# Kernel tuning notes

Hardware: AMD Instinct MI355X
Metric: run time of the kernel (lower is better)

## Reference

```python
import jax, jax.numpy as jnp
import numpy as np

CC_ITERS = 60  # min-label propagation + pointer doubling; covers huge diameters


def setup_inputs() -> dict:
    key = jax.random.key(0)
    k1, k2, k3, k4, k5 = jax.random.split(key, 5)
    N, C, E = 100000, 128, 800000
    x = jax.random.normal(k1, (N, C), jnp.float32)
    src = jax.random.randint(k2, (E,), 0, N)
    off = jax.random.randint(k3, (E,), 1, N)
    dst = (src + off) % N  # guarantees no self-loops (torch forward filters them)
    edge_index = jnp.stack([src, dst]).astype(jnp.int32)
    batch = jnp.zeros((N,), jnp.int32)
    W = jax.random.normal(k4, (2 * C,), jnp.float32) * 0.05
    b = (jax.random.normal(k5, (), jnp.float32) * 0.05).astype(jnp.float32)
    return {"x": x, "edge_index": edge_index, "batch": batch, "W": W, "b": b}


def _connected_components(src, dst, mask, N):
    # min-label propagation along selected edges, with path compression.
    def body(i, labels):
        ls = jnp.where(mask, labels[src], N)
        ld = jnp.where(mask, labels[dst], N)
        new = labels.at[dst].min(ls).at[src].min(ld)
        return jnp.minimum(new, new[new])  # pointer doubling
    return jax.lax.fori_loop(0, CC_ITERS, body, jnp.arange(N))


def reference(x, edge_index, batch, W, b):
    N, C = x.shape
    E = edge_index.shape[1]
    src, dst = edge_index[0], edge_index[1]

    # raw edge score: Linear(cat(x[src], x[dst])) without materializing the concat
    e = x[src] @ W[:C] + x[dst] @ W[C:] + b  # [E]
    # softmax over incoming edges of each dst node (segment softmax)
    m = jax.ops.segment_max(e, dst, num_segments=N)
    z = jnp.exp(e - m[dst])
    s = jax.ops.segment_sum(z, dst, num_segments=N)
    score = z / s[dst] + 0.5  # add_to_edge_score

    # edge selection (E > N -> quantile branch, matching torch)
    if E > N:
        q = 1.0 - (N // 2) / E
        mask = score > jnp.quantile(score, q)
    else:
        mask = score >= jnp.median(score)

    # weighted pairwise node reps for selected edges (masked instead of gathered)
    w = jnp.where(mask, score, 0.0)
    reps = (x[src] + x[dst]) * w[:, None]  # [E, C]
    mi = mask.astype(x.dtype)
    cnt = jnp.zeros((N,), x.dtype).at[src].add(mi).at[dst].add(mi)  # bincount of selected endpoints
    merged = cnt > 0
    base = jnp.where(merged[:, None], 0.0, x)  # merged nodes zeroed, untouched nodes keep x
    acc = base.at[src].add(reps).at[dst].add(reps)
    nodes = jnp.where(merged[:, None], acc / jnp.maximum(cnt, 1.0)[:, None], acc)

    # connected components over selected edges; relabel by first-occurrence order
    labels = _connected_components(src, dst, jax.lax.stop_gradient(mask), N)
    uniq = jnp.unique(labels, size=N, fill_value=N)
    cluster = jnp.searchsorted(uniq, labels)  # [N]

    new_x = jax.ops.segment_sum(nodes, cluster, num_segments=N)  # padded to N clusters

    # coalesce cluster-mapped edges: sorted unique pairs, padded with -1
    c0, c1 = cluster[src], cluster[dst]
    keys = jnp.unique(c0.astype(jnp.int64) * N + c1.astype(jnp.int64), size=E, fill_value=-1)
    valid = keys >= 0
    new_edge_index = jnp.stack([
        jnp.where(valid, keys // N, -1),
        jnp.where(valid, keys % N, -1),
    ])
    new_batch = jnp.zeros((N,), batch.dtype).at[cluster].set(batch)
    return new_x, new_edge_index, new_batch, score
```

## Files before the change

### kernel.cpp

```cpp
#include <hip/hip_runtime.h>
#include <math.h>
#include <stdint.h>

typedef unsigned long long u64;
typedef unsigned int u32;

#define NN 100000
#define CF 128
#define EE 800000

#define CAP 131072

#define EBITS 11
#define ERADIX 2048
#define ETILE 4096
#define NB_E 196
#define SORT_N (NB_E * ETILE)
#define MBITS 12
#define MRADIX 4096
#define MTILE 2048
#define NB_M 49
#define MSORT_N (NB_M * MTILE)
#define HISTG_LEN 401408

#define SCTILE 2048
#define MCHUNK 16

#define ZSCALE 4503599627370496.0
#define XSCALE 32768.0f
#define XINV   (1.0f / 32768.0f)

struct Sel { u32 prefix; u32 k; };

__device__ inline u64 encD(double v) {
  u64 u = (u64)__double_as_longlong(v);
  return u ^ ((u >> 63) ? ~0ULL : 0x8000000000000000ULL);
}
__device__ inline double decD(u64 u) {
  u ^= ((u >> 63) ? 0x8000000000000000ULL : ~0ULL);
  return __longlong_as_double((long long)u);
}

__global__ void k_pq(const float* __restrict__ x, const float* __restrict__ W,
                     double* __restrict__ p, double* __restrict__ q) {
  int node = blockIdx.x * 4 + (threadIdx.x >> 6);
  int lane = threadIdx.x & 63;
  if (node >= NN) return;
  const float* xr = x + (size_t)node * CF;
  double a = (double)xr[lane] * (double)W[lane] + (double)xr[lane + 64] * (double)W[lane + 64];
  double c = (double)xr[lane] * (double)W[CF + lane] + (double)xr[lane + 64] * (double)W[CF + lane + 64];
  for (int off = 32; off; off >>= 1) { a += __shfl_xor(a, off); c += __shfl_xor(c, off); }
  if (lane == 0) { p[node] = a; q[node] = c; }
}

__global__ void k_em(const int* __restrict__ ei, const double* __restrict__ p,
                     const double* __restrict__ q, const float* __restrict__ bptr,
                     double* __restrict__ e, u64* __restrict__ menc) {
  int j = blockIdx.x * 256 + threadIdx.x;
  if (j >= EE) return;
  int s = ei[j], d = ei[EE + j];
  double ev = p[s] + q[d] + (double)bptr[0];
  e[j] = ev;
  atomicMax(&menc[d], encD(ev));
}

__global__ void k_zs(const int* __restrict__ ei, double* __restrict__ e,
                     const u64* __restrict__ menc, u64* __restrict__ sdenFx) {
  int j = blockIdx.x * 256 + threadIdx.x;
  if (j >= EE) return;
  int d = ei[EE + j];
  double z = exp(e[j] - decD(menc[d]));
  e[j] = z;
  atomicAdd(&sdenFx[d], (u64)__double2ll_rn(z * ZSCALE));
}

__global__ void k_score(const int* __restrict__ ei, const double* __restrict__ z,
                        const u64* __restrict__ sdenFx, float* __restrict__ outScore) {
  int j = blockIdx.x * 256 + threadIdx.x;
  if (j >= EE) return;
  int d = ei[EE + j];
  double s = (double)sdenFx[d] * (1.0 / ZSCALE);
  outScore[j] = (float)(z[j] / s + 0.5);
}

__global__ void k_selInit(Sel* st, u32* hist, int k0, int k1) {
  int t = blockIdx.x * 256 + threadIdx.x;
  if (t == 0) { st[0].prefix = 0x3Fu; st[0].k = (u32)k0; st[1].prefix = 0x3Fu; st[1].k = (u32)k1; }
  if (t < 512) hist[t] = 0;
}

__global__ void k_selHist(const float* __restrict__ score, const Sel* __restrict__ st,
                          u32* __restrict__ hist, int shift) {
  __shared__ u32 h[512];
  for (int i = threadIdx.x; i < 512; i += 256) h[i] = 0;
  __syncthreads();
  u32 p0 = st[0].prefix, p1 = st[1].prefix;
  for (int j = blockIdx.x * 256 + threadIdx.x; j < EE; j += gridDim.x * 256) {
    u32 u = __float_as_uint(score[j]);
    u32 d = (u >> shift) & 255u;
    if ((u >> (shift + 8)) == p0) atomicAdd(&h[d], 1u);
    if ((u >> (shift + 8)) == p1) atomicAdd(&h[256 + d], 1u);
  }
  __syncthreads();
  for (int i = threadIdx.x; i < 512; i += 256) if (h[i]) atomicAdd(&hist[i], h[i]);
}

__global__ void k_selPick(Sel* st, u32* hist, float* tval, float frac, int last) {
  if (threadIdx.x == 0) {
    for (int sel = 0; sel < 2; sel++) {
      u32 k = st[sel].k, cum = 0;
      for (int b = 0; b < 256; b++) {
        u32 c = hist[sel * 256 + b];
        if (cum + c > k) { st[sel].prefix = (st[sel].prefix << 8) | (u32)b; st[sel].k = k - cum; break; }
        cum += c;
      }
    }
    if (last) {
      float a = __uint_as_float(st[0].prefix);
      float b = __uint_as_float(st[1].prefix);
      tval[0] = __fadd_rn(a, __fmul_rn(__fsub_rn(b, a), frac));
    }
  }
  __syncthreads();
  for (int i = threadIdx.x; i < 512; i += blockDim.x) hist[i] = 0;
}

__global__ void __launch_bounds__(1024) k_compact(
    const float* __restrict__ score, const float* __restrict__ tval,
    const int* __restrict__ ei, int* __restrict__ selCount,
    int* __restrict__ selSrc, int* __restrict__ selDst,
    float* __restrict__ selW, int* __restrict__ cnt, int* __restrict__ labels) {
  __shared__ int wbase[16];
  int j = blockIdx.x * 1024 + threadIdx.x;
  if (j < NN) labels[j] = j;
  int lane = threadIdx.x & 63;
  int wid = threadIdx.x >> 6;
  float sc = 0.0f;
  bool sel = false;
  if (j < EE) { sc = score[j]; sel = (sc > tval[0]); }
  u64 m = __ballot(sel);
  int wcnt = __popcll(m);
  int rank = __popcll(m & ((1ULL << lane) - 1ULL));
  if (lane == 0) wbase[wid] = wcnt;
  __syncthreads();
  if (threadIdx.x == 0) {
    int tot = 0;
#pragma unroll
    for (int w = 0; w < 16; w++) tot += wbase[w];
    int base = tot ? atomicAdd(selCount, tot) : 0;
#pragma unroll
    for (int w = 0; w < 16; w++) { int c = wbase[w]; wbase[w] = base; base += c; }
  }
  __syncthreads();
  if (sel) {
    int s = ei[j], d = ei[EE + j];
    int pos = wbase[wid] + rank;
    if (pos < CAP) { selSrc[pos] = s; selDst[pos] = d; selW[pos] = sc; }
    atomicAdd(&cnt[s], 1);
    atomicAdd(&cnt[d], 1);
  }
}

__device__ inline int uf_find(int* parent, int x) {
  while (true) {
    int p = parent[x];
    if (p == x) return x;
    int gp = parent[p];
    if (gp == p) return p;
    parent[x] = gp;
    x = gp;
  }
}

__global__ void k_ufUnion(const int* __restrict__ selSrc, const int* __restrict__ selDst,
                          const int* __restrict__ selCount, int* __restrict__ parent) {
  int n = selCount[0]; if (n > CAP) n = CAP;
  for (int e = blockIdx.x * 256 + threadIdx.x; e < n; e += gridDim.x * 256) {
    int ru = uf_find(parent, selSrc[e]);
    int rv = uf_find(parent, selDst[e]);
    while (ru != rv) {
      if (ru < rv) { int t = ru; ru = rv; rv = t; }
      int old = atomicCAS(&parent[ru], ru, rv);
      if (old == ru) break;
      ru = uf_find(parent, old);
      rv = uf_find(parent, rv);
    }
  }
}

__global__ void k_ufFlattenRoots(int* __restrict__ parent, int* __restrict__ roots) {
  int i = blockIdx.x * 256 + threadIdx.x;
  if (i >= NN) return;
  int x = i;
  while (true) { int p = parent[x]; if (p == x) break; x = p; }
  parent[i] = x;
  roots[i] = (x == i) ? 1 : 0;
}

__global__ void k_clusterMkeys(const int* __restrict__ labels, const int* __restrict__ rootScan,
                               int* __restrict__ cluster, u64* __restrict__ mkeys,
                               int* __restrict__ rootNode) {
  int i = blockIdx.x * 256 + threadIdx.x;
  if (i < NN) {
    int cl = rootScan[labels[i]];
    cluster[i] = cl;
    mkeys[i] = ((u64)(u32)cl << 32) | (u32)i;
    if (labels[i] == i) rootNode[cl] = i;
  } else if (i < MSORT_N) {
    mkeys[i] = ~0ULL;
  }
}

__global__ void k_scanBlock(const int* __restrict__ src, int* __restrict__ dst,
                            int n, int* __restrict__ bsums) {
  __shared__ int part[256];
  int base = blockIdx.x * SCTILE + threadIdx.x * 8;
  int v[8]; int s = 0;
#pragma unroll
  for (int i = 0; i < 8; i++) { v[i] = (base + i < n) ? src[base + i] : 0; s += v[i]; }
  part[threadIdx.x] = s;
  __syncthreads();
  for (int off = 1; off < 256; off <<= 1) {
    int t = (threadIdx.x >= off) ? part[threadIdx.x - off] : 0;
    __syncthreads();
    part[threadIdx.x] += t;
    __syncthreads();
  }
  int run = part[threadIdx.x] - s;
#pragma unroll
  for (int i = 0; i < 8; i++) { int vv = v[i]; if (base + i < n) dst[base + i] = run; run += vv; }
  if (threadIdx.x == 255) bsums[blockIdx.x] = part[255];
}
__global__ void k_scanFlags(const u32* __restrict__ keys, int* __restrict__ dst,
                            int n, int* __restrict__ bsums) {
  __shared__ int part[256];
  int base = blockIdx.x * SCTILE + threadIdx.x * 8;
  int v[8]; int s = 0;
#pragma unroll
  for (int i = 0; i < 8; i++) {
    int j = base + i;
    v[i] = (j < n) ? ((j == 0 || keys[j] != keys[j - 1]) ? 1 : 0) : 0;
    s += v[i];
  }
  part[threadIdx.x] = s;
  __syncthreads();
  for (int off = 1; off < 256; off <<= 1) {
    int t = (threadIdx.x >= off) ? part[threadIdx.x - off] : 0;
    __syncthreads();
    part[threadIdx.x] += t;
    __syncthreads();
  }
  int run = part[threadIdx.x] - s;
#pragma unroll
  for (int i = 0; i < 8; i++) { int vv = v[i]; if (base + i < n) dst[base + i] = run; run += vv; }
  if (threadIdx.x == 255) bsums[blockIdx.x] = part[255];
}
__global__ void k_scanTop(int* __restrict__ bsums, int nb) {
  __shared__ int part[256];
  int base = threadIdx.x * 4;
  int v[4]; int s = 0;
#pragma unroll
  for (int i = 0; i < 4; i++) { v[i] = (base + i < nb) ? bsums[base + i] : 0; s += v[i]; }
  part[threadIdx.x] = s;
  __syncthreads();
  for (int off = 1; off < 256; off <<= 1) {
    int t = (threadIdx.x >= off) ? part[threadIdx.x - off] : 0;
    __syncthreads();
    part[threadIdx.x] += t;
    __syncthreads();
  }
  int run = part[threadIdx.x] - s;
#pragma unroll
  for (int i = 0; i < 4; i++) { int vv = v[i]; if (base + i < nb) bsums[base + i] = run; run += vv; }
}
__global__ void k_scanAdd(int* __restrict__ data, int n, const int* __restrict__ bsums) {
  int add = bsums[blockIdx.x];
  int base = blockIdx.x * SCTILE + threadIdx.x * 8;
#pragma unroll
  for (int i = 0; i < 8; i++) if (base + i < n) data[base + i] += add;
}

template <typename K, int BITS, int TILE>
__global__ void k_sortHistT(const K* __restrict__ keys, int* __restrict__ hist,
                            int shift, int nb) {
  const int RAD = 1 << BITS;
  __shared__ int h[RAD];
  for (int i = threadIdx.x; i < RAD; i += 256) h[i] = 0;
  __syncthreads();
  int base = blockIdx.x * TILE;
  for (int i = threadIdx.x; i < TILE; i += 256) {
    int d = (int)((keys[base + i] >> shift) & (RAD - 1));
    atomicAdd(&h[d], 1);
  }
  __syncthreads();
  for (int i = threadIdx.x; i < RAD; i += 256) hist[i * nb + blockIdx.x] = h[i];
}

template <typename K, int BITS, int TILE>
__global__ void k_sortScatterT(const K* __restrict__ in, K* __restrict__ out,
                               const int* __restrict__ histScanned, int shift, int nb) {
  const int RAD = 1 << BITS;
  const int CH = TILE / 256;
  __shared__ int run[RAD];
  for (int i = threadIdx.x; i < RAD; i += 256) run[i] = 0;
  __syncthreads();
  int lane = threadIdx.x & 63;
  int wid = threadIdx.x >> 6;
  int base = blockIdx.x * TILE;
  for (int chunk = 0; chunk < CH; chunk++) {
    K key = in[base + chunk * 256 + threadIdx.x];
    int d = (int)((key >> shift) & (RAD - 1));
    u64 m = ~0ULL;
#pragma unroll
    for (int b = 0; b < BITS; b++) {
      u64 bal = __ballot((d >> b) & 1);
      m &= ((d >> b) & 1) ? bal : ~bal;
    }
    int laneRank = __popcll(m & ((1ULL << lane) - 1ULL));
    int cntm = __popcll(m);
    bool leader = (laneRank == 0);
    int local = 0;
    for (int w = 0; w < 4; w++) {
      if (wid == w) {
        int basev = run[d];
        local = basev + laneRank;
        if (leader) run[d] = basev + cntm;
      }
      __syncthreads();
    }
    out[histScanned[d * nb + blockIdx.x] + local] = key;
  }
}

__global__ void k_csr(const int* __restrict__ selSrc, const int* __restrict__ selDst,
                      const int* __restrict__ selCount, const int* __restrict__ nodeOff,
                      int* __restrict__ fill, int* __restrict__ edgeIdx) {
  int n = selCount[0]; if (n > CAP) n = CAP;
  for (int e = blockIdx.x * 256 + threadIdx.x; e < n; e += gridDim.x * 256) {
    int s = selSrc[e];
    int p = atomicAdd(&fill[s], 1);
    edgeIdx[nodeOff[s] + p] = e;
    int d = selDst[e];
    int p2 = atomicAdd(&fill[d], 1);
    edgeIdx[nodeOff[d] + p2] = e;
  }
}

__global__ void __launch_bounds__(128) k_clusterSum(
    const u64* __restrict__ mk, const int* __restrict__ nodeOff, const int* __restrict__ cnt,
    const int* __restrict__ edgeIdx, const int* __restrict__ selSrc,
    const int* __restrict__ selDst, const float* __restrict__ selW,
    const float* __restrict__ x, int* __restrict__ accX) {
  int c = threadIdx.x;
  int base = blockIdx.x * MCHUNK;
  if (base >= NN) return;
  int end = base + MCHUNK; if (end > NN) end = NN;
  u64 k0 = mk[base];
  int clN = (int)(k0 >> 32);
  int nodeN = (int)(k0 & 0xFFFFFFFFULL);
  int cntN = cnt[nodeN];
  int offN = nodeOff[nodeN];
  int curCl = -1; int acc = 0;
  for (int m = base; m < end; m++) {
    int cl = clN, ci = cntN, o = offN;
    if (m + 1 < end) {
      u64 k1 = mk[m + 1];
      clN = (int)(k1 >> 32);
      nodeN = (int)(k1 & 0xFFFFFFFFULL);
      cntN = cnt[nodeN];
      offN = nodeOff[nodeN];
    }
    if (ci == 0) continue;
    if (cl != curCl) {
      if (curCl >= 0 && acc != 0) atomicAdd(&accX[(size_t)curCl * CF + c], acc);
      curCl = cl; acc = 0;
    }
    int e0 = edgeIdx[o];
    float w = selW[e0];
    float xs = x[(size_t)selSrc[e0] * CF + c];
    float xd = x[(size_t)selDst[e0] * CF + c];
    for (int t = 0; t < ci; t++) {
      float cur = (xs + xd) * w;
      if (t + 1 < ci) {
        int e1 = edgeIdx[o + t + 1];
        w = selW[e1];
        xs = x[(size_t)selSrc[e1] * CF + c];
        xd = x[(size_t)selDst[e1] * CF + c];
      }
      acc += __float2int_rn((cur / (float)ci) * XSCALE);
    }
  }
  if (curCl >= 0 && acc != 0) atomicAdd(&accX[(size_t)curCl * CF + c], acc);
}

__global__ void k_finalFused(const float* __restrict__ x, const int* __restrict__ cnt,
                             const int* __restrict__ rootNode, const int* __restrict__ accX,
                             float* __restrict__ outNewX) {
  int t = (blockIdx.x * 256 + threadIdx.x) * 4;
  if (t >= NN * CF) return;
  int cl = t >> 7; int c = t & 127;
  int r = rootNode[cl];
  float4 o;
  if (r < 0) {
    o.x = o.y = o.z = o.w = 0.0f;
  } else if (cnt[r] == 0) {
    const float* xr = x + (size_t)r * CF + c;
    o.x = xr[0]; o.y = xr[1]; o.z = xr[2]; o.w = xr[3];
  } else {
    int4 v = *(const int4*)(accX + t);
    o.x = (float)v.x * XINV; o.y = (float)v.y * XINV;
    o.z = (float)v.z * XINV; o.w = (float)v.w * XINV;
  }
  *(float4*)(outNewX + t) = o;
}

__global__ void k_keysInit(const int* __restrict__ ei, const int* __restrict__ cluster,
                           u32* __restrict__ keys) {
  int t = blockIdx.x * 256 + threadIdx.x;
  if (t >= SORT_N) return;
  if (t < EE) {
    u32 kw = (u32)cluster[ei[t]] * 100000u + (u32)cluster[ei[EE + t]];
    keys[t] = kw ^ 0x80000000u;
  } else {
    keys[t] = 0xFFFFFFFFu;
  }
}

__global__ void k_eiFill(float* __restrict__ outEI) {
  int t = blockIdx.x * 256 + threadIdx.x;
  if (t < 2 * EE) outEI[t] = -1.0f;
}
__global__ void k_eiScatter(const u32* __restrict__ keys, const int* __restrict__ pos,
                            float* __restrict__ outEI) {
  int j = blockIdx.x * 256 + threadIdx.x;
  if (j >= EE) return;
  bool f = (j == 0 || keys[j] != keys[j - 1]);
  if (f) {
    int k32 = (int)(keys[j] ^ 0x80000000u);
    if (k32 >= 0) {
      int p = pos[j];
      outEI[p] = (float)(k32 / 100000);
      outEI[EE + p] = (float)(k32 % 100000);
    }
  }
}


static inline void runScan(int* data, int n, int* bsums, hipStream_t stream) {
  int nb = (n + SCTILE - 1) / SCTILE;
  k_scanBlock<<<nb, 256, 0, stream>>>(data, data, n, bsums);
  k_scanTop<<<1, 256, 0, stream>>>(bsums, nb);
  k_scanAdd<<<nb, 256, 0, stream>>>(data, n, bsums);
}
static inline void runScanFrom(const int* src, int* dst, int n, int* bsums, hipStream_t stream) {
  int nb = (n + SCTILE - 1) / SCTILE;
  k_scanBlock<<<nb, 256, 0, stream>>>(src, dst, n, bsums);
  k_scanTop<<<1, 256, 0, stream>>>(bsums, nb);
  k_scanAdd<<<nb, 256, 0, stream>>>(dst, n, bsums);
}

extern "C" void kernel_launch(void* const* d_in, const int* in_sizes, int n_in,
                              void* d_out, int out_size, void* d_ws, size_t ws_size,
                              hipStream_t stream) {
  const float* x = (const float*)d_in[0];
  const int* ei = (const int*)d_in[1];
  const float* W = (const float*)d_in[3];
  const float* bptr = (const float*)d_in[4];

  char* wp = (char*)d_ws;
  auto alloc = [&](size_t bytes) -> void* {
    void* r = (void*)wp;
    wp += (bytes + 255) & ~(size_t)255;
    return r;
  };
  double* ez = (double*)alloc((size_t)EE * 8);
  u32* sortA = (u32*)alloc((size_t)SORT_N * 4);
  u32* sortB = (u32*)alloc((size_t)SORT_N * 4);
  int* histG = (int*)alloc((size_t)HISTG_LEN * 4);
  int* fscan = (int*)alloc((size_t)EE * 4);
  double* p_d = (double*)alloc((size_t)NN * 8);
  double* q_d = (double*)alloc((size_t)NN * 8);
  u64* menc = (u64*)alloc((size_t)NN * 8);
  u64* sdenFx = (u64*)alloc((size_t)NN * 8);
  char* zeroAEnd = wp;
  int* accX = (int*)d_ws;
  const size_t ACCX_BYTES = (size_t)NN * CF * 4;
  if (wp < (char*)d_ws + ACCX_BYTES) wp = (char*)d_ws + ACCX_BYTES;
  int* cnt = (int*)alloc((size_t)NN * 4);
  int* fill = (int*)alloc((size_t)NN * 4);
  int* selCount = (int*)alloc(256);
  char* zeroBStart = (char*)cnt; char* zeroBEnd = wp;
  int* rootNode = (int*)alloc((size_t)NN * 4);
  int* nodeOff = (int*)alloc((size_t)NN * 4);
  int* selSrc = (int*)alloc((size_t)CAP * 4);
  int* selDst = (int*)alloc((size_t)CAP * 4);
  float* selW = (float*)alloc((size_t)CAP * 4);
  int* labels = (int*)alloc((size_t)NN * 4);
  int* cluster = (int*)alloc((size_t)NN * 4);
  int* edgeIdx = (int*)alloc((size_t)CAP * 4);
  u64* mA = (u64*)alloc((size_t)MSORT_N * 8);
  u64* mB = (u64*)alloc((size_t)MSORT_N * 8);
  int* bsums = (int*)alloc(1024 * 4);
  Sel* st = (Sel*)alloc(256);
  u32* selHist = (u32*)alloc(512 * 4);
  float* tval = (float*)alloc(256);
  (void)ws_size; (void)n_in; (void)in_sizes;

  float* outNewX = (float*)d_out;
  float* outEI = outNewX + (size_t)NN * CF;
  float* outBatch = outEI + 2 * (size_t)EE;
  float* outScore = outBatch + NN;

  double qd = 1.0 - (double)(NN / 2) / (double)EE;
  double posd = qd * (double)(EE - 1);
  int k0 = (int)floor(posd);
  double fracd = posd - floor(posd);
  int k1 = (fracd > 0.0) ? k0 + 1 : k0;
  float frac = (float)fracd;

  hipMemsetAsync(outBatch, 0, (size_t)NN * 4, stream);
  hipMemsetAsync(menc, 0, (size_t)(zeroAEnd - (char*)menc), stream);
  hipMemsetAsync(zeroBStart, 0, (size_t)(zeroBEnd - zeroBStart), stream);
  hipMemsetAsync(rootNode, 0xFF, (size_t)NN * 4, stream);

  k_pq<<<(NN + 3) / 4, 256, 0, stream>>>(x, W, p_d, q_d);
  k_em<<<(EE + 255) / 256, 256, 0, stream>>>(ei, p_d, q_d, bptr, ez, menc);
  k_zs<<<(EE + 255) / 256, 256, 0, stream>>>(ei, ez, menc, sdenFx);
  k_score<<<(EE + 255) / 256, 256, 0, stream>>>(ei, ez, sdenFx, outScore);

  k_selInit<<<2, 256, 0, stream>>>(st, selHist, k0, k1);
  for (int pass = 0; pass < 3; pass++) {
    k_selHist<<<1024, 256, 0, stream>>>(outScore, st, selHist, 16 - 8 * pass);
    k_selPick<<<1, 256, 0, stream>>>(st, selHist, tval, frac, pass == 2);
  }

  k_compact<<<(EE + 1023) / 1024, 1024, 0, stream>>>(outScore, tval, ei, selCount,
                                                     selSrc, selDst, selW, cnt, labels);

  k_ufUnion<<<256, 256, 0, stream>>>(selSrc, selDst, selCount, labels);
  k_ufUnion<<<256, 256, 0, stream>>>(selSrc, selDst, selCount, labels);
  k_ufFlattenRoots<<<(NN + 255) / 256, 256, 0, stream>>>(labels, fscan);

  runScan(fscan, NN, bsums, stream);
  k_clusterMkeys<<<(MSORT_N + 255) / 256, 256, 0, stream>>>(labels, fscan, cluster, mA, rootNode);

  {
    u64* msin = mA; u64* msout = mB;
    for (int pass = 0; pass < 2; pass++) {
      int shift = 32 + MBITS * pass;
      k_sortHistT<u64, MBITS, MTILE><<<NB_M, 256, 0, stream>>>(msin, histG, shift, NB_M);
      runScan(histG, MRADIX * NB_M, bsums, stream);
      k_sortScatterT<u64, MBITS, MTILE><<<NB_M, 256, 0, stream>>>(msin, msout, histG, shift, NB_M);
      u64* tmp = msin; msin = msout; msout = tmp;
    }
  }
  u64* memberKeys = mA;

  k_keysInit<<<SORT_N / 256, 256, 0, stream>>>(ei, cluster, sortA);
  u32* sin = sortA; u32* sout = sortB;
  for (int pass = 0; pass < 3; pass++) {
    int shift = EBITS * pass;
    k_sortHistT<u32, EBITS, ETILE><<<NB_E, 256, 0, stream>>>(sin, histG, shift, NB_E);
    runScan(histG, ERADIX * NB_E, bsums, stream);
    k_sortScatterT<u32, EBITS, ETILE><<<NB_E, 256, 0, stream>>>(sin, sout, histG, shift, NB_E);
    u32* tmp = sin; sin = sout; sout = tmp;
  }
  {
    int nb = (EE + SCTILE - 1) / SCTILE;
    k_scanFlags<<<nb, 256, 0, stream>>>(sin, fscan, EE, bsums);
    k_scanTop<<<1, 256, 0, stream>>>(bsums, nb);
    k_scanAdd<<<nb, 256, 0, stream>>>(fscan, EE, bsums);
  }
  k_eiFill<<<(2 * EE + 255) / 256, 256, 0, stream>>>(outEI);
  k_eiScatter<<<(EE + 255) / 256, 256, 0, stream>>>(sin, fscan, outEI);

  runScanFrom(cnt, nodeOff, NN, bsums, stream);
  k_csr<<<256, 256, 0, stream>>>(selSrc, selDst, selCount, nodeOff, fill, edgeIdx);

  hipMemsetAsync(accX, 0, ACCX_BYTES, stream);
  k_clusterSum<<<(NN + MCHUNK - 1) / MCHUNK, 128, 0, stream>>>(
      memberKeys, nodeOff, cnt, edgeIdx, selSrc, selDst, selW, x, accX);
  k_finalFused<<<(NN * CF / 4 + 255) / 256, 256, 0, stream>>>(x, cnt, rootNode, accX, outNewX);
}
```

Baseline: 686.1 us.

## Sort selected edges by cluster instead of nodes, drop CSR build, widen quantile radix

Cluster accumulation now iterates over selected edges sorted by the source endpoint's cluster, replacing the node-member sort plus CSR construction (scan, atomic fill, edgeIdx). Each edge adds its contribution divided by both endpoint counts. The quantile select moves from three 8-bit passes to two 12-bit passes with a parallel pick kernel, and the edge-index -1 fill is restricted to the tail past the unique count. This removes several kernel launches and a 100k-entry sort in exchange for sorting only about 64K edge keys. The destination's contribution is attributed to the source's cluster, which is only valid because both endpoints of a selected edge lie in the same component. The selected-edge count is capped at 65536 by the key packing.

```diff
diff --git a/kernel.cpp b/kernel.cpp
--- a/kernel.cpp
+++ b/kernel.cpp
@@ -16,15 +16,15 @@
 #define ETILE 4096
 #define NB_E 196
 #define SORT_N (NB_E * ETILE)
-#define MBITS 12
-#define MRADIX 4096
-#define MTILE 2048
-#define NB_M 49
-#define MSORT_N (NB_M * MTILE)
+#define KBITS 12
+#define KRADIX 4096
+#define KTILE 2048
+#define NB_EK 32
+#define EK_N (NB_EK * KTILE)
 #define HISTG_LEN 401408
 
 #define SCTILE 2048
-#define MCHUNK 16
+#define ECHUNK 16
 
 #define ZSCALE 4503599627370496.0
 #define XSCALE 32768.0f
@@ -86,43 +86,62 @@
 __global__ void k_selInit(Sel* st, u32* hist, int k0, int k1) {
   int t = blockIdx.x * 256 + threadIdx.x;
   if (t == 0) { st[0].prefix = 0x3Fu; st[0].k = (u32)k0; st[1].prefix = 0x3Fu; st[1].k = (u32)k1; }
-  if (t < 512) hist[t] = 0;
-}
-
-__global__ void k_selHist(const float* __restrict__ score, const Sel* __restrict__ st,
-                          u32* __restrict__ hist, int shift) {
-  __shared__ u32 h[512];
-  for (int i = threadIdx.x; i < 512; i += 256) h[i] = 0;
+  if (t < 2 * KRADIX) hist[t] = 0;
+}
+
+__global__ void k_selHist12(const float* __restrict__ score, const Sel* __restrict__ st,
+                            u32* __restrict__ hist, int shift) {
+  __shared__ u32 h[2 * KRADIX];
+  for (int i = threadIdx.x; i < 2 * KRADIX; i += 256) h[i] = 0;
   __syncthreads();
   u32 p0 = st[0].prefix, p1 = st[1].prefix;
   for (int j = blockIdx.x * 256 + threadIdx.x; j < EE; j += gridDim.x * 256) {
     u32 u = __float_as_uint(score[j]);
-    u32 d = (u >> shift) & 255u;
-    if ((u >> (shift + 8)) == p0) atomicAdd(&h[d], 1u);
-    if ((u >> (shift + 8)) == p1) atomicAdd(&h[256 + d], 1u);
-  }
-  __syncthreads();
-  for (int i = threadIdx.x; i < 512; i += 256) if (h[i]) atomicAdd(&hist[i], h[i]);
-}
-
-__global__ void k_selPick(Sel* st, u32* hist, float* tval, float frac, int last) {
-  if (threadIdx.x == 0) {
-    for (int sel = 0; sel < 2; sel++) {
-      u32 k = st[sel].k, cum = 0;
-      for (int b = 0; b < 256; b++) {
-        u32 c = hist[sel * 256 + b];
-        if (cum + c > k) { st[sel].prefix = (st[sel].prefix << 8) | (u32)b; st[sel].k = k - cum; break; }
-        cum += c;
+    u32 d = (u >> shift) & (KRADIX - 1);
+    if ((u >> (shift + 12)) == p0) atomicAdd(&h[d], 1u);
+    if ((u >> (shift + 12)) == p1) atomicAdd(&h[KRADIX + d], 1u);
+  }
+  __syncthreads();
+  for (int i = threadIdx.x; i < 2 * KRADIX; i += 256) if (h[i]) atomicAdd(&hist[i], h[i]);
+}
+
+__global__ void k_selPick12(Sel* st, u32* hist, float* tval, float frac, int last) {
+  __shared__ u32 part[256];
+  for (int sel = 0; sel < 2; sel++) {
+    u32 k = st[sel].k;
+    u32 loc[16]; u32 s = 0;
+    int base = sel * KRADIX + threadIdx.x * 16;
+#pragma unroll
+    for (int i = 0; i < 16; i++) { loc[i] = hist[base + i]; s += loc[i]; }
+    part[threadIdx.x] = s;
+    __syncthreads();
+    for (int off = 1; off < 256; off <<= 1) {
+      u32 t = (threadIdx.x >= off) ? part[threadIdx.x - off] : 0;
+      __syncthreads();
+      part[threadIdx.x] += t;
+      __syncthreads();
+    }
+    u32 excl = part[threadIdx.x] - s;
+    if (k >= excl && k < excl + s) {
+      u32 cum = excl;
+#pragma unroll
+      for (int i = 0; i < 16; i++) {
+        if (cum + loc[i] > k) {
+          st[sel].prefix = (st[sel].prefix << 12) | (u32)(threadIdx.x * 16 + i);
+          st[sel].k = k - cum;
+          break;
+        }
+        cum += loc[i];
       }
     }
-    if (last) {
-      float a = __uint_as_float(st[0].prefix);
-      float b = __uint_as_float(st[1].prefix);
-      tval[0] = __fadd_rn(a, __fmul_rn(__fsub_rn(b, a), frac));
-    }
-  }
-  __syncthreads();
-  for (int i = threadIdx.x; i < 512; i += blockDim.x) hist[i] = 0;
+    __syncthreads();
+  }
+  if (last && threadIdx.x == 0) {
+    float a = __uint_as_float(st[0].prefix);
+    float b = __uint_as_float(st[1].prefix);
+    tval[0] = __fadd_rn(a, __fmul_rn(__fsub_rn(b, a), frac));
+  }
+  for (int i = threadIdx.x; i < 2 * KRADIX; i += 256) hist[i] = 0;
 }
 
 __global__ void __launch_bounds__(1024) k_compact(
@@ -197,18 +216,13 @@
   roots[i] = (x == i) ? 1 : 0;
 }
 
-__global__ void k_clusterMkeys(const int* __restrict__ labels, const int* __restrict__ rootScan,
-                               int* __restrict__ cluster, u64* __restrict__ mkeys,
-                               int* __restrict__ rootNode) {
+__global__ void k_clusterRoot(const int* __restrict__ labels, const int* __restrict__ rootScan,
+                              int* __restrict__ cluster, int* __restrict__ rootNode) {
   int i = blockIdx.x * 256 + threadIdx.x;
-  if (i < NN) {
-    int cl = rootScan[labels[i]];
-    cluster[i] = cl;
-    mkeys[i] = ((u64)(u32)cl << 32) | (u32)i;
-    if (labels[i] == i) rootNode[cl] = i;
-  } else if (i < MSORT_N) {
-    mkeys[i] = ~0ULL;
-  }
+  if (i >= NN) return;
+  int cl = rootScan[labels[i]];
+  cluster[i] = cl;
+  if (labels[i] == i) rootNode[cl] = i;
 }
 
 __global__ void k_scanBlock(const int* __restrict__ src, int* __restrict__ dst,
@@ -332,65 +346,58 @@
   }
 }
 
-__global__ void k_csr(const int* __restrict__ selSrc, const int* __restrict__ selDst,
-                      const int* __restrict__ selCount, const int* __restrict__ nodeOff,
-                      int* __restrict__ fill, int* __restrict__ edgeIdx) {
-  int n = selCount[0]; if (n > CAP) n = CAP;
-  for (int e = blockIdx.x * 256 + threadIdx.x; e < n; e += gridDim.x * 256) {
-    int s = selSrc[e];
-    int p = atomicAdd(&fill[s], 1);
-    edgeIdx[nodeOff[s] + p] = e;
-    int d = selDst[e];
-    int p2 = atomicAdd(&fill[d], 1);
-    edgeIdx[nodeOff[d] + p2] = e;
-  }
-}
-
-__global__ void __launch_bounds__(128) k_clusterSum(
-    const u64* __restrict__ mk, const int* __restrict__ nodeOff, const int* __restrict__ cnt,
-    const int* __restrict__ edgeIdx, const int* __restrict__ selSrc,
+__global__ void k_ekeys(const int* __restrict__ selSrc, const int* __restrict__ cluster,
+                        const int* __restrict__ selCount, u64* __restrict__ keys) {
+  int t = blockIdx.x * 256 + threadIdx.x;
+  if (t >= EK_N) return;
+  int n = selCount[0]; if (n > EK_N) n = EK_N;
+  keys[t] = (t < n) ? (((u64)(u32)cluster[selSrc[t]] << 16) | (u32)t) : ~0ULL;
+}
+
+__global__ void __launch_bounds__(128) k_clusterSum2(
+    const u64* __restrict__ ek, const int* __restrict__ selSrc,
     const int* __restrict__ selDst, const float* __restrict__ selW,
-    const float* __restrict__ x, int* __restrict__ accX) {
+    const int* __restrict__ cnt, const float* __restrict__ x, int* __restrict__ accX) {
   int c = threadIdx.x;
-  int base = blockIdx.x * MCHUNK;
-  if (base >= NN) return;
-  int end = base + MCHUNK; if (end > NN) end = NN;
-  u64 k0 = mk[base];
-  int clN = (int)(k0 >> 32);
-  int nodeN = (int)(k0 & 0xFFFFFFFFULL);
-  int cntN = cnt[nodeN];
-  int offN = nodeOff[nodeN];
-  int curCl = -1; int acc = 0;
+  int base = blockIdx.x * ECHUNK;
+  u64 kc = ek[base];
+  if (kc == ~0ULL) return;
+  int cc = (int)(kc >> 16);
+  int e0 = (int)(kc & 0xFFFF);
+  int s0 = selSrc[e0], d0 = selDst[e0];
+  float wN = selW[e0];
+  float xsN = x[(size_t)s0 * CF + c];
+  float xdN = x[(size_t)d0 * CF + c];
+  int csN = cnt[s0], cdN = cnt[d0];
+  int curCl = cc;
+  int acc = 0;
+  int end = base + ECHUNK;
   for (int m = base; m < end; m++) {
-    int cl = clN, ci = cntN, o = offN;
+    int cl = cc; float w = wN, xs = xsN, xd = xdN; int cs = csN, cd = cdN;
+    bool last = true;
     if (m + 1 < end) {
-      u64 k1 = mk[m + 1];
-      clN = (int)(k1 >> 32);
-      nodeN = (int)(k1 & 0xFFFFFFFFULL);
-      cntN = cnt[nodeN];
-      offN = nodeOff[nodeN];
-    }
-    if (ci == 0) continue;
+      u64 kn = ek[m + 1];
+      if (kn != ~0ULL) {
+        last = false;
+        cc = (int)(kn >> 16);
+        int e1 = (int)(kn & 0xFFFF);
+        int s1 = selSrc[e1], d1 = selDst[e1];
+        wN = selW[e1];
+        xsN = x[(size_t)s1 * CF + c];
+        xdN = x[(size_t)d1 * CF + c];
+        csN = cnt[s1]; cdN = cnt[d1];
+      }
+    }
     if (cl != curCl) {
-      if (curCl >= 0 && acc != 0) atomicAdd(&accX[(size_t)curCl * CF + c], acc);
+      if (acc != 0) atomicAdd(&accX[(size_t)curCl * CF + c], acc);
       curCl = cl; acc = 0;
     }
-    int e0 = edgeIdx[o];
-    float w = selW[e0];
-    float xs = x[(size_t)selSrc[e0] * CF + c];
-    float xd = x[(size_t)selDst[e0] * CF + c];
-    for (int t = 0; t < ci; t++) {
-      float cur = (xs + xd) * w;
-      if (t + 1 < ci) {
-        int e1 = edgeIdx[o + t + 1];
-        w = selW[e1];
-        xs = x[(size_t)selSrc[e1] * CF + c];
-        xd = x[(size_t)selDst[e1] * CF + c];
-      }
-      acc += __float2int_rn((cur / (float)ci) * XSCALE);
-    }
-  }
-  if (curCl >= 0 && acc != 0) atomicAdd(&accX[(size_t)curCl * CF + c], acc);
+    float r = (xs + xd) * w;
+    acc += __float2int_rn((r / (float)cs) * XSCALE)
+         + __float2int_rn((r / (float)cd) * XSCALE);
+    if (last) break;
+  }
+  if (acc != 0) atomicAdd(&accX[(size_t)curCl * CF + c], acc);
 }
 
 __global__ void k_finalFused(const float* __restrict__ x, const int* __restrict__ cnt,
@@ -426,23 +433,32 @@
   }
 }
 
-__global__ void k_eiFill(float* __restrict__ outEI) {
-  int t = blockIdx.x * 256 + threadIdx.x;
-  if (t < 2 * EE) outEI[t] = -1.0f;
-}
 __global__ void k_eiScatter(const u32* __restrict__ keys, const int* __restrict__ pos,
                             float* __restrict__ outEI) {
   int j = blockIdx.x * 256 + threadIdx.x;
   if (j >= EE) return;
   bool f = (j == 0 || keys[j] != keys[j - 1]);
   if (f) {
+    int p = pos[j];
     int k32 = (int)(keys[j] ^ 0x80000000u);
     if (k32 >= 0) {
-      int p = pos[j];
       outEI[p] = (float)(k32 / 100000);
       outEI[EE + p] = (float)(k32 % 100000);
-    }
-  }
+    } else {
+      outEI[p] = -1.0f;
+      outEI[EE + p] = -1.0f;
+    }
+  }
+}
+__global__ void k_eiTail(const int* __restrict__ fscan, const u32* __restrict__ keys,
+                         float* __restrict__ outEI) {
+  __shared__ int sU;
+  if (threadIdx.x == 0)
+    sU = fscan[EE - 1] + ((keys[EE - 1] != keys[EE - 2]) ? 1 : 0);
+  __syncthreads();
+  int U = sU;
+  int p = blockIdx.x * 256 + threadIdx.x;
+  if (p < EE && p >= U) { outEI[p] = -1.0f; outEI[EE + p] = -1.0f; }
 }
 
 
@@ -451,12 +467,6 @@
   k_scanBlock<<<nb, 256, 0, stream>>>(data, data, n, bsums);
   k_scanTop<<<1, 256, 0, stream>>>(bsums, nb);
   k_scanAdd<<<nb, 256, 0, stream>>>(data, n, bsums);
-}
-static inline void runScanFrom(const int* src, int* dst, int n, int* bsums, hipStream_t stream) {
-  int nb = (n + SCTILE - 1) / SCTILE;
-  k_scanBlock<<<nb, 256, 0, stream>>>(src, dst, n, bsums);
-  k_scanTop<<<1, 256, 0, stream>>>(bsums, nb);
-  k_scanAdd<<<nb, 256, 0, stream>>>(dst, n, bsums);
 }
 
 extern "C" void kernel_launch(void* const* d_in, const int* in_sizes, int n_in,
@@ -487,22 +497,19 @@
   const size_t ACCX_BYTES = (size_t)NN * CF * 4;
   if (wp < (char*)d_ws + ACCX_BYTES) wp = (char*)d_ws + ACCX_BYTES;
   int* cnt = (int*)alloc((size_t)NN * 4);
-  int* fill = (int*)alloc((size_t)NN * 4);
   int* selCount = (int*)alloc(256);
   char* zeroBStart = (char*)cnt; char* zeroBEnd = wp;
   int* rootNode = (int*)alloc((size_t)NN * 4);
-  int* nodeOff = (int*)alloc((size_t)NN * 4);
   int* selSrc = (int*)alloc((size_t)CAP * 4);
   int* selDst = (int*)alloc((size_t)CAP * 4);
   float* selW = (float*)alloc((size_t)CAP * 4);
   int* labels = (int*)alloc((size_t)NN * 4);
   int* cluster = (int*)alloc((size_t)NN * 4);
-  int* edgeIdx = (int*)alloc((size_t)CAP * 4);
-  u64* mA = (u64*)alloc((size_t)MSORT_N * 8);
-  u64* mB = (u64*)alloc((size_t)MSORT_N * 8);
+  u64* ekA = (u64*)alloc((size_t)EK_N * 8);
+  u64* ekB = (u64*)alloc((size_t)EK_N * 8);
   int* bsums = (int*)alloc(1024 * 4);
   Sel* st = (Sel*)alloc(256);
-  u32* selHist = (u32*)alloc(512 * 4);
+  u32* selHist = (u32*)alloc((size_t)2 * KRADIX * 4);
   float* tval = (float*)alloc(256);
   (void)ws_size; (void)n_in; (void)in_sizes;
 
@@ -528,10 +535,10 @@
   k_zs<<<(EE + 255) / 256, 256, 0, stream>>>(ei, ez, menc, sdenFx);
   k_score<<<(EE + 255) / 256, 256, 0, stream>>>(ei, ez, sdenFx, outScore);
 
-  k_selInit<<<2, 256, 0, stream>>>(st, selHist, k0, k1);
-  for (int pass = 0; pass < 3; pass++) {
-    k_selHist<<<1024, 256, 0, stream>>>(outScore, st, selHist, 16 - 8 * pass);
-    k_selPick<<<1, 256, 0, stream>>>(st, selHist, tval, frac, pass == 2);
+  k_selInit<<<(2 * KRADIX + 255) / 256, 256, 0, stream>>>(st, selHist, k0, k1);
+  for (int pass = 0; pass < 2; pass++) {
+    k_selHist12<<<1024, 256, 0, stream>>>(outScore, st, selHist, 12 - 12 * pass);
+    k_selPick12<<<1, 256, 0, stream>>>(st, selHist, tval, frac, pass == 1);
   }
 
   k_compact<<<(EE + 1023) / 1024, 1024, 0, stream>>>(outScore, tval, ei, selCount,
@@ -542,19 +549,19 @@
   k_ufFlattenRoots<<<(NN + 255) / 256, 256, 0, stream>>>(labels, fscan);
 
   runScan(fscan, NN, bsums, stream);
-  k_clusterMkeys<<<(MSORT_N + 255) / 256, 256, 0, stream>>>(labels, fscan, cluster, mA, rootNode);
-
+  k_clusterRoot<<<(NN + 255) / 256, 256, 0, stream>>>(labels, fscan, cluster, rootNode);
+
+  k_ekeys<<<EK_N / 256, 256, 0, stream>>>(selSrc, cluster, selCount, ekA);
   {
-    u64* msin = mA; u64* msout = mB;
+    u64* kin = ekA; u64* kout = ekB;
     for (int pass = 0; pass < 2; pass++) {
-      int shift = 32 + MBITS * pass;
-      k_sortHistT<u64, MBITS, MTILE><<<NB_M, 256, 0, stream>>>(msin, histG, shift, NB_M);
-      runScan(histG, MRADIX * NB_M, bsums, stream);
-      k_sortScatterT<u64, MBITS, MTILE><<<NB_M, 256, 0, stream>>>(msin, msout, histG, shift, NB_M);
-      u64* tmp = msin; msin = msout; msout = tmp;
-    }
-  }
-  u64* memberKeys = mA;
+      int shift = 16 + KBITS * pass;
+      k_sortHistT<u64, KBITS, KTILE><<<NB_EK, 256, 0, stream>>>(kin, histG, shift, NB_EK);
+      runScan(histG, KRADIX * NB_EK, bsums, stream);
+      k_sortScatterT<u64, KBITS, KTILE><<<NB_EK, 256, 0, stream>>>(kin, kout, histG, shift, NB_EK);
+      u64* tmp = kin; kin = kout; kout = tmp;
+    }
+  }
 
   k_keysInit<<<SORT_N / 256, 256, 0, stream>>>(ei, cluster, sortA);
   u32* sin = sortA; u32* sout = sortB;
@@ -571,14 +578,10 @@
     k_scanTop<<<1, 256, 0, stream>>>(bsums, nb);
     k_scanAdd<<<nb, 256, 0, stream>>>(fscan, EE, bsums);
   }
-  k_eiFill<<<(2 * EE + 255) / 256, 256, 0, stream>>>(outEI);
   k_eiScatter<<<(EE + 255) / 256, 256, 0, stream>>>(sin, fscan, outEI);
-
-  runScanFrom(cnt, nodeOff, NN, bsums, stream);
-  k_csr<<<256, 256, 0, stream>>>(selSrc, selDst, selCount, nodeOff, fill, edgeIdx);
+  k_eiTail<<<(EE + 255) / 256, 256, 0, stream>>>(fscan, sin, outEI);
 
   hipMemsetAsync(accX, 0, ACCX_BYTES, stream);
-  k_clusterSum<<<(NN + MCHUNK - 1) / MCHUNK, 128, 0, stream>>>(
-      memberKeys, nodeOff, cnt, edgeIdx, selSrc, selDst, selW, x, accX);
+  k_clusterSum2<<<EK_N / ECHUNK, 128, 0, stream>>>(ekA, selSrc, selDst, selW, cnt, x, accX);
   k_finalFused<<<(NN * CF / 4 + 255) / 256, 256, 0, stream>>>(x, cnt, rootNode, accX, outNewX);
 }
```

After: 596.1 us. 13.1% less time.
